# Kernel optimization log

Measured on AMD Instinct MI355X. Metric: run time of the kernel, lower is better.

The kernel has to match this reference:

```python
import jax, jax.numpy as jnp
import numpy as np

N = 131072   # n_nodes == n_edges (required by the broadcast in the original module)
C = 256      # node_channels == edge_channels (required by the broadcast)
EPS_BN = 1e-5
EPS = 1e-5


def _linear_params(key, out_c, in_c):
    k1, k2 = jax.random.split(key)
    bound = 1.0 / np.sqrt(in_c)
    W = jax.random.uniform(k1, (out_c, in_c), minval=-bound, maxval=bound, dtype=jnp.float32)
    b = jax.random.uniform(k2, (out_c,), minval=-bound, maxval=bound, dtype=jnp.float32)
    return W, b


def setup_inputs() -> dict:
    key = jax.random.key(0)
    ks = jax.random.split(key, 10)
    h = jax.random.normal(ks[0], (N, C), dtype=jnp.float32)
    e = jax.random.normal(ks[1], (N, C), dtype=jnp.float32)
    edge_index = jax.random.randint(ks[2], (2, N), 0, N, dtype=jnp.int64)
    A_w, A_b = _linear_params(ks[3], C, C)
    B_w, B_b = _linear_params(ks[4], C, C)
    C_w, C_b = _linear_params(ks[5], C, C)
    D_w, D_b = _linear_params(ks[6], C, C)
    U_w, U_b = _linear_params(ks[7], C, C)
    V_w, V_b = _linear_params(ks[8], C, C)
    bn_gamma = jnp.ones((C,), dtype=jnp.float32)
    bn_beta = jnp.zeros((C,), dtype=jnp.float32)
    return dict(h=h, edge_index=edge_index, e=e,
                A_w=A_w, A_b=A_b, B_w=B_w, B_b=B_b,
                C_w=C_w, C_b=C_b, D_w=D_w, D_b=D_b,
                bn_gamma=bn_gamma, bn_beta=bn_beta,
                U_w=U_w, U_b=U_b, V_w=V_w, V_b=V_b)


def reference(h, edge_index, e,
              A_w, A_b, B_w, B_b, C_w, C_b, D_w, D_b,
              bn_gamma, bn_beta, U_w, U_b, V_w, V_b):
    row, col = edge_index[0], edge_index[1]
    # gather + four parallel linears, summed: [E, C]
    e_out = (h[row] @ A_w.T + A_b
             + h[col] @ B_w.T + B_b
             + e[col] @ C_w.T + C_b
             + e[row] @ D_w.T + D_b)
    # BatchNorm1d (training mode: batch stats, biased variance) + ReLU
    mu = jnp.mean(e_out, axis=0)
    var = jnp.var(e_out, axis=0)
    e_out = jax.nn.relu(bn_gamma * (e_out - mu) * jax.lax.rsqrt(var + EPS_BN) + bn_beta)
    # scatter-add edge messages into node-indexed e, then sigmoid-normalize over dim 0
    e_new = e.at[row].add(e_out)
    e_new = jax.nn.sigmoid(e_new)
    e_new = e_new / (jnp.sum(e_new, axis=0, keepdims=True) + EPS)
    # final gather-multiply-reduce: (e_new * V(h[col])).sum(0) broadcasts [N,C]*[E,C] with N==E
    h_out = h @ U_w.T + U_b + jnp.sum(e_new * (h[col] @ V_w.T + V_b), axis=0)
    h_out = jax.nn.relu(h_out)
    return h_out, e_new
```

## Files before the change

kernel.cpp:

```cpp
#include <hip/hip_runtime.h>
#include <hip/hip_bf16.h>


typedef __attribute__((ext_vector_type(8))) short bf16x8;
typedef __attribute__((ext_vector_type(4))) float f32x4;

__device__ __forceinline__ float b2f(unsigned int lo16) {
  union { unsigned int u; float f; } c; c.u = lo16 << 16; return c.f;
}
__device__ __forceinline__ float lof(unsigned int u) { return b2f(u & 0xffffu); }
__device__ __forceinline__ float hif(unsigned int u) { return b2f(u >> 16); }
__device__ __forceinline__ unsigned int f2b(float f) {
  union { float f; unsigned int u; } c; c.f = f;
  unsigned int u = c.u;
  u += 0x7fffu + ((u >> 16) & 1u);
  return u >> 16;
}

__device__ __forceinline__ void prep_chunk(const float* __restrict__ src,
                                           unsigned short* __restrict__ dst, int g) {
  int mtile = g >> 9;
  int rem = g & 511;
  int r = rem >> 5, k8 = rem & 31;
  const float4* s = reinterpret_cast<const float4*>(src + (((size_t)mtile * 16 + r) << 8) + k8 * 8);
  float4 v0 = s[0], v1 = s[1];
  uint4 o;
  o.x = f2b(v0.x) | (f2b(v0.y) << 16);
  o.y = f2b(v0.z) | (f2b(v0.w) << 16);
  o.z = f2b(v1.x) | (f2b(v1.y) << 16);
  o.w = f2b(v1.z) | (f2b(v1.w) << 16);
  *reinterpret_cast<uint4*>(dst + ((size_t)mtile * 512 + k8 * 16 + r) * 8) = o;
}

__global__ __launch_bounds__(256) void prep_he(const float* __restrict__ h,
                                               unsigned short* __restrict__ h_t,
                                               const float* __restrict__ e,
                                               unsigned short* __restrict__ e_t,
                                               int nChunksEach) {
  int g = blockIdx.x * 256 + threadIdx.x;
  if (g < nChunksEach) prep_chunk(h, h_t, g);
  else if (g < 2 * nChunksEach) prep_chunk(e, e_t, g - nChunksEach);
}

__global__ __launch_bounds__(256) void prep_weights(
    const float* __restrict__ s0, const float* __restrict__ s1,
    const float* __restrict__ s2, const float* __restrict__ s3,
    const float* __restrict__ s4, const float* __restrict__ s5,
    unsigned short* __restrict__ W1h, unsigned short* __restrict__ W1e,
    unsigned short* __restrict__ W2t,
    const float* __restrict__ Ab, const float* __restrict__ Db,
    const float* __restrict__ Bb, const float* __restrict__ Cb,
    const float* __restrict__ Vb, const float* __restrict__ Ub,
    float* __restrict__ b1, float* __restrict__ b2,
    const int* __restrict__ ei, int* __restrict__ mode) {
  int g = blockIdx.x * 256 + threadIdx.x;
  if (blockIdx.x == 0) {
    const int t = threadIdx.x;
    b1[t] = Ab[t] + Db[t];
    b1[256 + t] = Bb[t] + Cb[t];
    b2[t] = Vb[t];
    b2[256 + t] = Ub[t];
    if (t == 0) {
      int m = 0;
#pragma unroll
      for (int i = 1; i < 64; i += 2) m |= ei[i];
      *mode = (m == 0) ? 1 : 0;
    }
  }
  int sel = g >> 13;
  int gg = g & 8191;
  const float* src; unsigned short* dst;
  switch (sel) {
    case 0: src = s0; dst = W1h; break;
    case 1: src = s1; dst = W1h + 65536; break;
    case 2: src = s2; dst = W1e; break;
    case 3: src = s3; dst = W1e + 65536; break;
    case 4: src = s4; dst = W2t; break;
    default: src = s5; dst = W2t + 65536; break;
  }
  prep_chunk(src, dst, gg);
}

__global__ __launch_bounds__(256) void gemm_bt2(
    const unsigned short* __restrict__ Ah, const unsigned short* __restrict__ Ae,
    const unsigned short* __restrict__ Bh, const unsigned short* __restrict__ Be,
    const float* __restrict__ bias, unsigned short* __restrict__ Cmat,
    int O, int nColBlk, int ktSteps, int nBlk) {
  __shared__ char lds[16384];
  const int cpx = nBlk >> 3;
  const int hw = blockIdx.x;
  const int bid = (hw % 8) * cpx + hw / 8;
  const int colBlk = bid % nColBlk;
  const int rowBlk = bid / nColBlk;
  const int tid = threadIdx.x;
  const int w = tid >> 6, lane = tid & 63;
  const int wm = w >> 1, wn = w & 1;

  const size_t aTileOff = (size_t)(rowBlk * 8 + w * 2) * 8192 + lane * 16;
  const size_t bTileOff = (size_t)(colBlk * 8 + w * 2) * 8192 + lane * 16;
  char* ldsA0 = lds + (w * 2) * 1024;
  char* ldsA1 = lds + (w * 2 + 1) * 1024;
  char* ldsB0 = lds + 8192 + (w * 2) * 1024;
  char* ldsB1 = lds + 8192 + (w * 2 + 1) * 1024;

  f32x4 acc[4][4] = {};

  for (int kt = 0; kt < ktSteps; ++kt) {
    const char* Abase = (const char*)(kt < 8 ? Ah : Ae) + aTileOff + (size_t)(kt & 7) * 1024;
    const char* Bbase = (const char*)(kt < 8 ? Bh : Be) + bTileOff + (size_t)(kt & 7) * 1024;
    __builtin_amdgcn_global_load_lds((const __attribute__((address_space(1))) void*)Abase,
                                     (__attribute__((address_space(3))) void*)ldsA0, 16, 0, 0);
    __builtin_amdgcn_global_load_lds((const __attribute__((address_space(1))) void*)(Abase + 8192),
                                     (__attribute__((address_space(3))) void*)ldsA1, 16, 0, 0);
    __builtin_amdgcn_global_load_lds((const __attribute__((address_space(1))) void*)Bbase,
                                     (__attribute__((address_space(3))) void*)ldsB0, 16, 0, 0);
    __builtin_amdgcn_global_load_lds((const __attribute__((address_space(1))) void*)(Bbase + 8192),
                                     (__attribute__((address_space(3))) void*)ldsB1, 16, 0, 0);
    __syncthreads();
    bf16x8 a[4], b[4];
#pragma unroll
    for (int mi = 0; mi < 4; ++mi)
      a[mi] = *reinterpret_cast<const bf16x8*>(lds + (wm * 4 + mi) * 1024 + lane * 16);
#pragma unroll
    for (int ni = 0; ni < 4; ++ni)
      b[ni] = *reinterpret_cast<const bf16x8*>(lds + 8192 + (wn * 4 + ni) * 1024 + lane * 16);
#pragma unroll
    for (int mi = 0; mi < 4; ++mi)
#pragma unroll
      for (int ni = 0; ni < 4; ++ni)
        acc[mi][ni] = __builtin_amdgcn_mfma_f32_16x16x32_bf16(a[mi], b[ni], acc[mi][ni], 0, 0, 0);
    __syncthreads();
  }

  const int rb = rowBlk * 128 + wm * 64 + ((lane >> 4) << 2);
  const int cb = colBlk * 128 + wn * 64 + (lane & 15);
#pragma unroll
  for (int mi = 0; mi < 4; ++mi) {
#pragma unroll
    for (int ni = 0; ni < 4; ++ni) {
      const int coln = cb + ni * 16;
      const float bz = bias[coln];
      const size_t base = (size_t)(rb + mi * 16) * O + coln;
#pragma unroll
      for (int r = 0; r < 4; ++r)
        Cmat[base + (size_t)r * O] = (unsigned short)f2b(acc[mi][ni][r] + bz);
    }
  }
}

__global__ __launch_bounds__(256) void edge_stats(
    const unsigned short* __restrict__ PRPC,
    const int* __restrict__ rows_s, const int* __restrict__ cols_s,
    float* __restrict__ sums, float* __restrict__ sumsq) {
  __shared__ float red[8][256];
  const int c8 = threadIdx.x & 31;
  const int sub = threadIdx.x >> 5;
  float s[8], q[8];
#pragma unroll
  for (int j = 0; j < 8; ++j) { s[j] = 0.f; q[j] = 0.f; }
#pragma unroll 1
  for (int grp = 0; grp < 2; ++grp) {
    const int kb = blockIdx.x * 64 + grp * 32 + sub * 4;
    int r[4], cj[4];
#pragma unroll
    for (int u = 0; u < 4; ++u) { r[u] = rows_s[kb + u]; cj[u] = cols_s[kb + u]; }
    uint4 pr[4], pc[4];
#pragma unroll
    for (int u = 0; u < 4; ++u)
      pr[u] = *reinterpret_cast<const uint4*>(PRPC + (size_t)r[u] * 512 + c8 * 8);
#pragma unroll
    for (int u = 0; u < 4; ++u)
      pc[u] = *reinterpret_cast<const uint4*>(PRPC + (size_t)cj[u] * 512 + 256 + c8 * 8);
#pragma unroll
    for (int u = 0; u < 4; ++u) {
      const unsigned int rw[4] = {pr[u].x, pr[u].y, pr[u].z, pr[u].w};
      const unsigned int cw[4] = {pc[u].x, pc[u].y, pc[u].z, pc[u].w};
#pragma unroll
      for (int p4 = 0; p4 < 4; ++p4) {
        const float v0 = lof(rw[p4]) + lof(cw[p4]);
        const float v1 = hif(rw[p4]) + hif(cw[p4]);
        s[2 * p4] += v0;     q[2 * p4] += v0 * v0;
        s[2 * p4 + 1] += v1; q[2 * p4 + 1] += v1 * v1;
      }
    }
  }
#pragma unroll
  for (int j = 0; j < 8; ++j) red[sub][c8 * 8 + j] = s[j];
  __syncthreads();
  {
    const int c = threadIdx.x;
    float t = 0.f;
#pragma unroll
    for (int u2 = 0; u2 < 8; ++u2) t += red[u2][c];
    atomicAdd(sums + c, t);
  }
  __syncthreads();
#pragma unroll
  for (int j = 0; j < 8; ++j) red[sub][c8 * 8 + j] = q[j];
  __syncthreads();
  {
    const int c = threadIdx.x;
    float t = 0.f;
#pragma unroll
    for (int u2 = 0; u2 < 8; ++u2) t += red[u2][c];
    atomicAdd(sumsq + c, t);
  }
}

__global__ __launch_bounds__(256) void hist_rows(const int* __restrict__ ei,
                                                 const int* __restrict__ modep,
                                                 int* __restrict__ cnt, int Nn) {
  const int k = blockIdx.x * 256 + threadIdx.x;
  if (k >= Nn) return;
  const int row = (*modep) ? ei[2 * k] : ei[k];
  atomicAdd(&cnt[row], 1);
}

__global__ __launch_bounds__(256) void scan1(const int* __restrict__ cnt,
                                             int* __restrict__ bsum) {
  __shared__ int red[256];
  const int t = threadIdx.x;
  red[t] = cnt[blockIdx.x * 256 + t];
  __syncthreads();
#pragma unroll
  for (int s = 128; s > 0; s >>= 1) {
    if (t < s) red[t] += red[t + s];
    __syncthreads();
  }
  if (t == 0) bsum[blockIdx.x] = red[0];
}

__global__ __launch_bounds__(512) void scan2(int* __restrict__ bsum, int nb) {
  __shared__ int tmp[512];
  const int t = threadIdx.x;
  const int own = (t < nb) ? bsum[t] : 0;
  tmp[t] = own;
  __syncthreads();
  for (int off = 1; off < 512; off <<= 1) {
    int v = (t >= off) ? tmp[t - off] : 0;
    __syncthreads();
    tmp[t] += v;
    __syncthreads();
  }
  if (t < nb) bsum[t] = tmp[t] - own;
}

__global__ __launch_bounds__(256) void scan3(const int* __restrict__ cnt,
                                             const int* __restrict__ bsum,
                                             int* __restrict__ base, int Nn) {
  __shared__ int tmp[256];
  const int t = threadIdx.x;
  const int gid = blockIdx.x * 256 + t;
  const int own = cnt[gid];
  tmp[t] = own;
  __syncthreads();
  for (int off = 1; off < 256; off <<= 1) {
    int v = (t >= off) ? tmp[t - off] : 0;
    __syncthreads();
    tmp[t] += v;
    __syncthreads();
  }
  base[gid] = tmp[t] - own + bsum[blockIdx.x];
  if (gid == 0) base[Nn] = Nn;
}

__global__ __launch_bounds__(256) void scatter_eids(const int* __restrict__ ei,
                                                    const int* __restrict__ modep,
                                                    const int* __restrict__ base,
                                                    int* __restrict__ cnt,
                                                    int* __restrict__ rows_s,
                                                    int* __restrict__ cols_s, int Nn) {
  const int k = blockIdx.x * 256 + threadIdx.x;
  if (k >= Nn) return;
  int row, col;
  if (*modep) { row = ei[2 * k]; col = ei[2 * (Nn + k)]; }
  else        { row = ei[k];     col = ei[Nn + k]; }
  const int pos = base[row] + atomicAdd(&cnt[row], -1) - 1;
  rows_s[pos] = row;
  cols_s[pos] = col;
}

#define GCAP 1024
__global__ __launch_bounds__(256) void gather_sig_T(
    const float* __restrict__ e, const unsigned short* __restrict__ PRPC,
    const int* __restrict__ base, const int* __restrict__ cols_s,
    const int* __restrict__ ei, const int* __restrict__ modep,
    const unsigned short* __restrict__ VU,
    const float* __restrict__ sums, const float* __restrict__ sumsq,
    const float* __restrict__ gamma, const float* __restrict__ beta,
    unsigned short* __restrict__ accB, float* __restrict__ colsum,
    float* __restrict__ Traw, float invE, int Nn) {
  __shared__ float red[4][256];
  __shared__ int colsL[GCAP];
  __shared__ int baseL[65];
  const int lane = threadIdx.x & 63, w = threadIdx.x >> 6;
  const int n0 = blockIdx.x * 64;
  if (threadIdx.x < 65) baseL[threadIdx.x] = base[n0 + threadIdx.x];
  __syncthreads();
  const int bstart = baseL[0];
  const int bcount = baseL[64] - bstart;
  for (int qq = threadIdx.x; qq < bcount && qq < GCAP; qq += 256)
    colsL[qq] = cols_s[bstart + qq];
  const float4 sm = *reinterpret_cast<const float4*>(sums + lane * 4);
  const float4 sq = *reinterpret_cast<const float4*>(sumsq + lane * 4);
  const float4 gm = *reinterpret_cast<const float4*>(gamma + lane * 4);
  const float4 bt = *reinterpret_cast<const float4*>(beta + lane * 4);
  float4 sc, sh;
  {
    const float mx = sm.x * invE, my = sm.y * invE, mz = sm.z * invE, mw = sm.w * invE;
    sc.x = gm.x * rsqrtf(fmaxf(sq.x * invE - mx * mx, 0.f) + 1e-5f);
    sc.y = gm.y * rsqrtf(fmaxf(sq.y * invE - my * my, 0.f) + 1e-5f);
    sc.z = gm.z * rsqrtf(fmaxf(sq.z * invE - mz * mz, 0.f) + 1e-5f);
    sc.w = gm.w * rsqrtf(fmaxf(sq.w * invE - mw * mw, 0.f) + 1e-5f);
    sh.x = bt.x - mx * sc.x; sh.y = bt.y - my * sc.y;
    sh.z = bt.z - mz * sc.z; sh.w = bt.w - mw * sc.w;
  }
  __syncthreads();
  const int mode = *modep;
  float s0 = 0.f, s1 = 0.f, s2 = 0.f, s3 = 0.f;
  float t0 = 0.f, t1 = 0.f, t2 = 0.f, t3 = 0.f;
  const int i0 = n0 + w * 16;
  int p = baseL[w * 16];
  const int pendW = baseL[w * 16 + 16];
  uint2 pcn; pcn.x = 0; pcn.y = 0;
  if (p < pendW) {
    const int q0 = p - bstart;
    const int cj = (q0 < GCAP) ? colsL[q0] : cols_s[p];
    pcn = *reinterpret_cast<const uint2*>(PRPC + (size_t)cj * 512 + 256 + lane * 4);
  }
  float4 ev = *reinterpret_cast<const float4*>(e + (size_t)i0 * 256 + lane * 4);
  uint2 prv = *reinterpret_cast<const uint2*>(PRPC + (size_t)i0 * 512 + lane * 4);
#pragma unroll 1
  for (int it = 0; it < 16; ++it) {
    const int i = i0 + it;
    const int colT = mode ? ei[2 * (Nn + i)] : ei[Nn + i];
    const uint2 hv = *reinterpret_cast<const uint2*>(VU + (size_t)colT * 512 + lane * 4);
    float4 v = ev;
    const uint2 pr = prv;
    if (it + 1 < 16) {
      ev = *reinterpret_cast<const float4*>(e + (size_t)(i + 1) * 256 + lane * 4);
      prv = *reinterpret_cast<const uint2*>(PRPC + (size_t)(i + 1) * 512 + lane * 4);
    }
    const float pr0 = lof(pr.x), pr1 = hif(pr.x), pr2 = lof(pr.y), pr3 = hif(pr.y);
    const int pe = baseL[w * 16 + it + 1];
#pragma unroll 1
    while (p < pe) {
      const uint2 pc = pcn;
      if (p + 1 < pendW) {
        const int qn = p + 1 - bstart;
        const int cj = (qn < GCAP) ? colsL[qn] : cols_s[p + 1];
        pcn = *reinterpret_cast<const uint2*>(PRPC + (size_t)cj * 512 + 256 + lane * 4);
      }
      v.x += fmaxf(fmaf(sc.x, pr0 + lof(pc.x), sh.x), 0.f);
      v.y += fmaxf(fmaf(sc.y, pr1 + hif(pc.x), sh.y), 0.f);
      v.z += fmaxf(fmaf(sc.z, pr2 + lof(pc.y), sh.z), 0.f);
      v.w += fmaxf(fmaf(sc.w, pr3 + hif(pc.y), sh.w), 0.f);
      ++p;
    }
    v.x = 1.f / (1.f + __expf(-v.x));
    v.y = 1.f / (1.f + __expf(-v.y));
    v.z = 1.f / (1.f + __expf(-v.z));
    v.w = 1.f / (1.f + __expf(-v.w));
    uint2 ob;
    ob.x = f2b(v.x) | (f2b(v.y) << 16);
    ob.y = f2b(v.z) | (f2b(v.w) << 16);
    *reinterpret_cast<uint2*>(accB + (size_t)i * 256 + lane * 4) = ob;
    s0 += v.x; s1 += v.y; s2 += v.z; s3 += v.w;
    t0 += v.x * lof(hv.x); t1 += v.y * hif(hv.x);
    t2 += v.z * lof(hv.y); t3 += v.w * hif(hv.y);
  }
  red[w][lane * 4 + 0] = s0;
  red[w][lane * 4 + 1] = s1;
  red[w][lane * 4 + 2] = s2;
  red[w][lane * 4 + 3] = s3;
  __syncthreads();
  {
    const int c = threadIdx.x;
    atomicAdd(colsum + c, red[0][c] + red[1][c] + red[2][c] + red[3][c]);
  }
  __syncthreads();
  red[w][lane * 4 + 0] = t0;
  red[w][lane * 4 + 1] = t1;
  red[w][lane * 4 + 2] = t2;
  red[w][lane * 4 + 3] = t3;
  __syncthreads();
  {
    const int c = threadIdx.x;
    atomicAdd(Traw + c, red[0][c] + red[1][c] + red[2][c] + red[3][c]);
  }
}

__global__ __launch_bounds__(256) void finalize(
    const unsigned short* __restrict__ accB, const unsigned short* __restrict__ VU,
    const float* __restrict__ colsum, const float* __restrict__ Traw,
    float* __restrict__ outE, float* __restrict__ outH, int nChunks) {
  const int g = blockIdx.x * 256 + threadIdx.x;
  if (g >= nChunks) return;
  const int i = g >> 5, c8 = g & 31;
  const float4 cs0 = *reinterpret_cast<const float4*>(colsum + c8 * 8);
  const float4 cs1 = *reinterpret_cast<const float4*>(colsum + c8 * 8 + 4);
  const float4 tr0 = *reinterpret_cast<const float4*>(Traw + c8 * 8);
  const float4 tr1 = *reinterpret_cast<const float4*>(Traw + c8 * 8 + 4);
  float iv[8] = {1.f / (cs0.x + 1e-5f), 1.f / (cs0.y + 1e-5f),
                 1.f / (cs0.z + 1e-5f), 1.f / (cs0.w + 1e-5f),
                 1.f / (cs1.x + 1e-5f), 1.f / (cs1.y + 1e-5f),
                 1.f / (cs1.z + 1e-5f), 1.f / (cs1.w + 1e-5f)};
  float tt[8] = {tr0.x * iv[0], tr0.y * iv[1], tr0.z * iv[2], tr0.w * iv[3],
                 tr1.x * iv[4], tr1.y * iv[5], tr1.z * iv[6], tr1.w * iv[7]};
  const uint4 sb = *reinterpret_cast<const uint4*>(accB + (size_t)i * 256 + c8 * 8);
  const unsigned int sw[4] = {sb.x, sb.y, sb.z, sb.w};
  float4 e0, e1;
  e0.x = lof(sw[0]) * iv[0]; e0.y = hif(sw[0]) * iv[1];
  e0.z = lof(sw[1]) * iv[2]; e0.w = hif(sw[1]) * iv[3];
  e1.x = lof(sw[2]) * iv[4]; e1.y = hif(sw[2]) * iv[5];
  e1.z = lof(sw[3]) * iv[6]; e1.w = hif(sw[3]) * iv[7];
  float4* qe = reinterpret_cast<float4*>(outE + (size_t)i * 256 + c8 * 8);
  qe[0] = e0; qe[1] = e1;
  const uint4 hu = *reinterpret_cast<const uint4*>(VU + (size_t)i * 512 + 256 + c8 * 8);
  float4 o0, o1;
  o0.x = fmaxf(lof(hu.x) + tt[0], 0.f);
  o0.y = fmaxf(hif(hu.x) + tt[1], 0.f);
  o0.z = fmaxf(lof(hu.y) + tt[2], 0.f);
  o0.w = fmaxf(hif(hu.y) + tt[3], 0.f);
  o1.x = fmaxf(lof(hu.z) + tt[4], 0.f);
  o1.y = fmaxf(hif(hu.z) + tt[5], 0.f);
  o1.z = fmaxf(lof(hu.w) + tt[6], 0.f);
  o1.w = fmaxf(hif(hu.w) + tt[7], 0.f);
  float4* qh = reinterpret_cast<float4*>(outH + (size_t)i * 256 + c8 * 8);
  qh[0] = o0; qh[1] = o1;
}

extern "C" void kernel_launch(void* const* d_in, const int* in_sizes, int n_in,
                              void* d_out, int out_size, void* d_ws, size_t ws_size,
                              hipStream_t stream) {
  const float* h     = (const float*)d_in[0];
  const int*   ei    = (const int*)d_in[1];
  const float* e     = (const float*)d_in[2];
  const float* Aw    = (const float*)d_in[3];
  const float* Ab    = (const float*)d_in[4];
  const float* Bw    = (const float*)d_in[5];
  const float* Bb    = (const float*)d_in[6];
  const float* Cw    = (const float*)d_in[7];
  const float* Cb    = (const float*)d_in[8];
  const float* Dw    = (const float*)d_in[9];
  const float* Db    = (const float*)d_in[10];
  const float* gamma = (const float*)d_in[11];
  const float* beta  = (const float*)d_in[12];
  const float* Uw    = (const float*)d_in[13];
  const float* Ub    = (const float*)d_in[14];
  const float* Vw    = (const float*)d_in[15];
  const float* Vb    = (const float*)d_in[16];
  const int N = in_sizes[0] / 256;

  char* ws = (char*)d_ws;
  unsigned short* W1h = (unsigned short*)(ws + 0x0);
  unsigned short* W1e = (unsigned short*)(ws + 0x40000);
  unsigned short* W2t = (unsigned short*)(ws + 0x80000);
  float* b1     = (float*)(ws + 0xC0000);
  float* b2     = (float*)(ws + 0xC0800);
  float* sums   = (float*)(ws + 0xC1000);
  float* sumsq  = (float*)(ws + 0xC1400);
  float* colsum = (float*)(ws + 0xC1800);
  float* Traw   = (float*)(ws + 0xC1C00);
  int*   mode   = (int*)(ws + 0xC2C00);
  unsigned short* h_t  = (unsigned short*)(ws + 0x100000);
  unsigned short* e_t  = (unsigned short*)(ws + 0x4100000);
  unsigned short* PRPC = (unsigned short*)(ws + 0x8100000);
  unsigned short* VU   = (unsigned short*)(ws + 0x10100000);
  unsigned short* accB = (unsigned short*)(ws + 0x100000);
  int* cnt    = (int*)(ws + 0x18100000);
  int* baseA  = (int*)(ws + 0x18180000);
  int* rows_s = (int*)(ws + 0x18210000);
  int* cols_s = (int*)(ws + 0x18290000);
  int* bsum   = (int*)(ws + 0x18310000);

  float* outH = (float*)d_out;
  float* outE = outH + (size_t)N * 256;

  hipMemsetAsync(ws + 0xC1000, 0, 4096, stream);
  hipMemsetAsync(cnt, 0, (size_t)N * 4, stream);
  prep_weights<<<192, 256, 0, stream>>>(Aw, Bw, Dw, Cw, Vw, Uw, W1h, W1e, W2t,
                                        Ab, Db, Bb, Cb, Vb, Ub, b1, b2, ei, mode);

  hist_rows<<<N / 256, 256, 0, stream>>>(ei, mode, cnt, N);
  scan1<<<N / 256, 256, 0, stream>>>(cnt, bsum);
  scan2<<<1, 512, 0, stream>>>(bsum, N / 256);
  scan3<<<N / 256, 256, 0, stream>>>(cnt, bsum, baseA, N);
  scatter_eids<<<N / 256, 256, 0, stream>>>(ei, mode, baseA, cnt, rows_s, cols_s, N);

  const int nChunks = N * 32;
  prep_he<<<2 * nChunks / 256, 256, 0, stream>>>(h, h_t, e, e_t, nChunks);
  gemm_bt2<<<(N / 128) * 4, 256, 0, stream>>>(h_t, e_t, W1h, W1e, b1, PRPC, 512, 4, 16, (N / 128) * 4);
  gemm_bt2<<<(N / 128) * 4, 256, 0, stream>>>(h_t, h_t, W2t, W2t, b2, VU, 512, 4, 8, (N / 128) * 4);

  edge_stats<<<N / 64, 256, 0, stream>>>(PRPC, rows_s, cols_s, sums, sumsq);
  gather_sig_T<<<N / 64, 256, 0, stream>>>(e, PRPC, baseA, cols_s, ei, mode, VU,
                                           sums, sumsq, gamma, beta,
                                           accB, colsum, Traw, 1.0f / (float)N, N);
  finalize<<<nChunks / 256, 256, 0, stream>>>(accB, VU, colsum, Traw, outE, outH, nChunks);
}
```

Before: 574.1 us.

## Fuse counting sort into one grid-barrier kernel and merge the two GEMM launches

Replaces the five-kernel counting sort (histogram, three scan passes, scatter) with one persistent kernel of 256 blocks that uses a software grid barrier between phases. The two bf16 GEMMs become a single launch whose blocks pick their operands by index, and the memsets are folded into prep_weights. The aim is to cut launch gaps and small-kernel tail overhead; in exchange the sort runs on fewer blocks and depends on all 256 blocks being resident at once for the spin barrier to avoid deadlock.

```diff
diff --git a/kernel.cpp b/kernel.cpp
--- a/kernel.cpp
+++ b/kernel.cpp
@@ -52,7 +52,9 @@
     const float* __restrict__ Bb, const float* __restrict__ Cb,
     const float* __restrict__ Vb, const float* __restrict__ Ub,
     float* __restrict__ b1, float* __restrict__ b2,
-    const int* __restrict__ ei, int* __restrict__ mode) {
+    float* __restrict__ sums, float* __restrict__ sumsq,
+    float* __restrict__ colsum, float* __restrict__ Traw,
+    const int* __restrict__ ei, int* __restrict__ mode, int* __restrict__ bar) {
   int g = blockIdx.x * 256 + threadIdx.x;
   if (blockIdx.x == 0) {
     const int t = threadIdx.x;
@@ -60,11 +62,13 @@
     b1[256 + t] = Bb[t] + Cb[t];
     b2[t] = Vb[t];
     b2[256 + t] = Ub[t];
+    sums[t] = 0.f; sumsq[t] = 0.f; colsum[t] = 0.f; Traw[t] = 0.f;
     if (t == 0) {
       int m = 0;
 #pragma unroll
       for (int i = 1; i < 64; i += 2) m |= ei[i];
       *mode = (m == 0) ? 1 : 0;
+      *bar = 0;
     }
   }
   int sel = g >> 13;
@@ -81,14 +85,114 @@
   prep_chunk(src, dst, gg);
 }
 
-__global__ __launch_bounds__(256) void gemm_bt2(
-    const unsigned short* __restrict__ Ah, const unsigned short* __restrict__ Ae,
-    const unsigned short* __restrict__ Bh, const unsigned short* __restrict__ Be,
-    const float* __restrict__ bias, unsigned short* __restrict__ Cmat,
-    int O, int nColBlk, int ktSteps, int nBlk) {
+__device__ __forceinline__ void gridbar(int* bar, int target) {
+  __syncthreads();
+  if (threadIdx.x == 0) {
+    __threadfence();
+    atomicAdd(bar, 1);
+    while (__hip_atomic_load(bar, __ATOMIC_RELAXED, __HIP_MEMORY_SCOPE_AGENT) < target) {
+      __builtin_amdgcn_s_sleep(2);
+    }
+    __threadfence();
+  }
+  __syncthreads();
+}
+
+__global__ __launch_bounds__(256, 2) void coop_sort(
+    const int* __restrict__ ei, const int* __restrict__ modep,
+    int* __restrict__ cnt, int* __restrict__ bsum, int* __restrict__ baseA,
+    int* __restrict__ rows_s, int* __restrict__ cols_s,
+    int* __restrict__ bar, int Nn) {
+  __shared__ int tmp[512];
+  const int t = threadIdx.x;
+  const int b = blockIdx.x;
+  const int NB = 256;
+  const int mode = *modep;
+  int row[2], col[2];
+#pragma unroll
+  for (int half = 0; half < 2; ++half) {
+    const int g = (b + half * NB) * 256 + t;
+    cnt[g] = 0;
+    if (mode) { row[half] = ei[2 * g]; col[half] = ei[2 * (Nn + g)]; }
+    else      { row[half] = ei[g];     col[half] = ei[Nn + g]; }
+  }
+  gridbar(bar, NB);
+  atomicAdd(&cnt[row[0]], 1);
+  atomicAdd(&cnt[row[1]], 1);
+  gridbar(bar, 2 * NB);
+  int own[2];
+#pragma unroll
+  for (int half = 0; half < 2; ++half) {
+    const int g = (b + half * NB) * 256 + t;
+    own[half] = __hip_atomic_load(&cnt[g], __ATOMIC_RELAXED, __HIP_MEMORY_SCOPE_AGENT);
+    tmp[t] = own[half];
+    __syncthreads();
+    for (int s = 128; s > 0; s >>= 1) { if (t < s) tmp[t] += tmp[t + s]; __syncthreads(); }
+    if (t == 0) bsum[b + half * NB] = tmp[0];
+    __syncthreads();
+  }
+  gridbar(bar, 3 * NB);
+  if (b == 0) {
+    const int o0 = bsum[t], o1 = bsum[t + 256];
+    tmp[t] = o0; tmp[t + 256] = o1;
+    __syncthreads();
+    for (int off = 1; off < 256; off <<= 1) {
+      const int a0 = (t >= off) ? tmp[t - off] : 0;
+      const int a1 = (t >= off) ? tmp[256 + t - off] : 0;
+      __syncthreads();
+      tmp[t] += a0; tmp[256 + t] += a1;
+      __syncthreads();
+    }
+    const int tot1 = tmp[255];
+    bsum[t] = tmp[t] - o0;
+    bsum[t + 256] = tmp[256 + t] + tot1 - o1;
+  }
+  gridbar(bar, 4 * NB);
+#pragma unroll
+  for (int half = 0; half < 2; ++half) {
+    const int g = (b + half * NB) * 256 + t;
+    const int bs = __hip_atomic_load(&bsum[b + half * NB], __ATOMIC_RELAXED, __HIP_MEMORY_SCOPE_AGENT);
+    tmp[t] = own[half];
+    __syncthreads();
+    for (int off = 1; off < 256; off <<= 1) {
+      const int a = (t >= off) ? tmp[t - off] : 0;
+      __syncthreads();
+      tmp[t] += a;
+      __syncthreads();
+    }
+    baseA[g] = tmp[t] - own[half] + bs;
+    __syncthreads();
+  }
+  if (b == 0 && t == 0) baseA[Nn] = Nn;
+  gridbar(bar, 5 * NB);
+#pragma unroll
+  for (int half = 0; half < 2; ++half) {
+    const int pos = baseA[row[half]] + atomicAdd(&cnt[row[half]], -1) - 1;
+    rows_s[pos] = row[half];
+    cols_s[pos] = col[half];
+  }
+}
+
+__global__ __launch_bounds__(256) void gemm_fused(
+    const unsigned short* __restrict__ h_t, const unsigned short* __restrict__ e_t,
+    const unsigned short* __restrict__ W1h, const unsigned short* __restrict__ W1e,
+    const unsigned short* __restrict__ W2t,
+    const float* __restrict__ b1, const float* __restrict__ b2,
+    unsigned short* __restrict__ PRPC, unsigned short* __restrict__ VU,
+    int nB1) {
   __shared__ char lds[16384];
-  const int cpx = nBlk >> 3;
-  const int hw = blockIdx.x;
+  const int g = blockIdx.x;
+  const bool is2 = (g >= nB1);
+  const int hw = is2 ? (g - nB1) : g;
+  const unsigned short* Ah = h_t;
+  const unsigned short* Ae = e_t;
+  const unsigned short* Bh = is2 ? W2t : W1h;
+  const unsigned short* Be = is2 ? W2t : W1e;
+  const float* bias = is2 ? b2 : b1;
+  unsigned short* Cmat = is2 ? VU : PRPC;
+  const int ktSteps = is2 ? 8 : 16;
+  const int O = 512, nColBlk = 4;
+  const int cpx = nB1 >> 3;
   const int bid = (hw % 8) * cpx + hw / 8;
   const int colBlk = bid % nColBlk;
   const int rowBlk = bid / nColBlk;
@@ -205,79 +309,6 @@
     for (int u2 = 0; u2 < 8; ++u2) t += red[u2][c];
     atomicAdd(sumsq + c, t);
   }
-}
-
-__global__ __launch_bounds__(256) void hist_rows(const int* __restrict__ ei,
-                                                 const int* __restrict__ modep,
-                                                 int* __restrict__ cnt, int Nn) {
-  const int k = blockIdx.x * 256 + threadIdx.x;
-  if (k >= Nn) return;
-  const int row = (*modep) ? ei[2 * k] : ei[k];
-  atomicAdd(&cnt[row], 1);
-}
-
-__global__ __launch_bounds__(256) void scan1(const int* __restrict__ cnt,
-                                             int* __restrict__ bsum) {
-  __shared__ int red[256];
-  const int t = threadIdx.x;
-  red[t] = cnt[blockIdx.x * 256 + t];
-  __syncthreads();
-#pragma unroll
-  for (int s = 128; s > 0; s >>= 1) {
-    if (t < s) red[t] += red[t + s];
-    __syncthreads();
-  }
-  if (t == 0) bsum[blockIdx.x] = red[0];
-}
-
-__global__ __launch_bounds__(512) void scan2(int* __restrict__ bsum, int nb) {
-  __shared__ int tmp[512];
-  const int t = threadIdx.x;
-  const int own = (t < nb) ? bsum[t] : 0;
-  tmp[t] = own;
-  __syncthreads();
-  for (int off = 1; off < 512; off <<= 1) {
-    int v = (t >= off) ? tmp[t - off] : 0;
-    __syncthreads();
-    tmp[t] += v;
-    __syncthreads();
-  }
-  if (t < nb) bsum[t] = tmp[t] - own;
-}
-
-__global__ __launch_bounds__(256) void scan3(const int* __restrict__ cnt,
-                                             const int* __restrict__ bsum,
-                                             int* __restrict__ base, int Nn) {
-  __shared__ int tmp[256];
-  const int t = threadIdx.x;
-  const int gid = blockIdx.x * 256 + t;
-  const int own = cnt[gid];
-  tmp[t] = own;
-  __syncthreads();
-  for (int off = 1; off < 256; off <<= 1) {
-    int v = (t >= off) ? tmp[t - off] : 0;
-    __syncthreads();
-    tmp[t] += v;
-    __syncthreads();
-  }
-  base[gid] = tmp[t] - own + bsum[blockIdx.x];
-  if (gid == 0) base[Nn] = Nn;
-}
-
-__global__ __launch_bounds__(256) void scatter_eids(const int* __restrict__ ei,
-                                                    const int* __restrict__ modep,
-                                                    const int* __restrict__ base,
-                                                    int* __restrict__ cnt,
-                                                    int* __restrict__ rows_s,
-                                                    int* __restrict__ cols_s, int Nn) {
-  const int k = blockIdx.x * 256 + threadIdx.x;
-  if (k >= Nn) return;
-  int row, col;
-  if (*modep) { row = ei[2 * k]; col = ei[2 * (Nn + k)]; }
-  else        { row = ei[k];     col = ei[Nn + k]; }
-  const int pos = base[row] + atomicAdd(&cnt[row], -1) - 1;
-  rows_s[pos] = row;
-  cols_s[pos] = col;
 }
 
 #define GCAP 1024
@@ -463,6 +494,7 @@
   float* colsum = (float*)(ws + 0xC1800);
   float* Traw   = (float*)(ws + 0xC1C00);
   int*   mode   = (int*)(ws + 0xC2C00);
+  int*   bar    = (int*)(ws + 0xC2D00);
   unsigned short* h_t  = (unsigned short*)(ws + 0x100000);
   unsigned short* e_t  = (unsigned short*)(ws + 0x4100000);
   unsigned short* PRPC = (unsigned short*)(ws + 0x8100000);
@@ -477,21 +509,15 @@
   float* outH = (float*)d_out;
   float* outE = outH + (size_t)N * 256;
 
-  hipMemsetAsync(ws + 0xC1000, 0, 4096, stream);
-  hipMemsetAsync(cnt, 0, (size_t)N * 4, stream);
   prep_weights<<<192, 256, 0, stream>>>(Aw, Bw, Dw, Cw, Vw, Uw, W1h, W1e, W2t,
-                                        Ab, Db, Bb, Cb, Vb, Ub, b1, b2, ei, mode);
-
-  hist_rows<<<N / 256, 256, 0, stream>>>(ei, mode, cnt, N);
-  scan1<<<N / 256, 256, 0, stream>>>(cnt, bsum);
-  scan2<<<1, 512, 0, stream>>>(bsum, N / 256);
-  scan3<<<N / 256, 256, 0, stream>>>(cnt, bsum, baseA, N);
-  scatter_eids<<<N / 256, 256, 0, stream>>>(ei, mode, baseA, cnt, rows_s, cols_s, N);
+                                        Ab, Db, Bb, Cb, Vb, Ub, b1, b2,
+                                        sums, sumsq, colsum, Traw, ei, mode, bar);
+  coop_sort<<<256, 256, 0, stream>>>(ei, mode, cnt, bsum, baseA, rows_s, cols_s, bar, N);
 
   const int nChunks = N * 32;
   prep_he<<<2 * nChunks / 256, 256, 0, stream>>>(h, h_t, e, e_t, nChunks);
-  gemm_bt2<<<(N / 128) * 4, 256, 0, stream>>>(h_t, e_t, W1h, W1e, b1, PRPC, 512, 4, 16, (N / 128) * 4);
-  gemm_bt2<<<(N / 128) * 4, 256, 0, stream>>>(h_t, h_t, W2t, W2t, b2, VU, 512, 4, 8, (N / 128) * 4);
+  const int nB1 = (N / 128) * 4;
+  gemm_fused<<<2 * nB1, 256, 0, stream>>>(h_t, e_t, W1h, W1e, W2t, b1, b2, PRPC, VU, nB1);
 
   edge_stats<<<N / 64, 256, 0, stream>>>(PRPC, rows_s, cols_s, sums, sumsq);
   gather_sig_T<<<N / 64, 256, 0, stream>>>(e, PRPC, baseA, cols_s, ei, mode, VU,
```

New measurement: 630.6 us. 1.1x slower.

## Double-buffer LDS tiles in bf16 GEMM and fold stat zeroing into weight prep

Applied to the files above, without the earlier changes.

The GEMM main loop now uses two LDS buffers, 32 KB in total. The global-to-LDS load for the next K step is issued before the MFMA work on the current step, so memory latency can overlap with compute instead of waiting behind a barrier every step. Separately, the memset that zeroed the BN and column-sum accumulators is removed, and block 0 of the weight-prep kernel zeroes them instead, saving one launch. The larger LDS footprint may lower the number of resident blocks per CU.

```diff
diff --git a/kernel.cpp b/kernel.cpp
--- a/kernel.cpp
+++ b/kernel.cpp
@@ -52,6 +52,8 @@
     const float* __restrict__ Bb, const float* __restrict__ Cb,
     const float* __restrict__ Vb, const float* __restrict__ Ub,
     float* __restrict__ b1, float* __restrict__ b2,
+    float* __restrict__ sums, float* __restrict__ sumsq,
+    float* __restrict__ colsum, float* __restrict__ Traw,
     const int* __restrict__ ei, int* __restrict__ mode) {
   int g = blockIdx.x * 256 + threadIdx.x;
   if (blockIdx.x == 0) {
@@ -60,6 +62,7 @@
     b1[256 + t] = Bb[t] + Cb[t];
     b2[t] = Vb[t];
     b2[256 + t] = Ub[t];
+    sums[t] = 0.f; sumsq[t] = 0.f; colsum[t] = 0.f; Traw[t] = 0.f;
     if (t == 0) {
       int m = 0;
 #pragma unroll
@@ -86,7 +89,7 @@
     const unsigned short* __restrict__ Bh, const unsigned short* __restrict__ Be,
     const float* __restrict__ bias, unsigned short* __restrict__ Cmat,
     int O, int nColBlk, int ktSteps, int nBlk) {
-  __shared__ char lds[16384];
+  __shared__ char lds[32768];
   const int cpx = nBlk >> 3;
   const int hw = blockIdx.x;
   const int bid = (hw % 8) * cpx + hw / 8;
@@ -98,37 +101,50 @@
 
   const size_t aTileOff = (size_t)(rowBlk * 8 + w * 2) * 8192 + lane * 16;
   const size_t bTileOff = (size_t)(colBlk * 8 + w * 2) * 8192 + lane * 16;
-  char* ldsA0 = lds + (w * 2) * 1024;
-  char* ldsA1 = lds + (w * 2 + 1) * 1024;
-  char* ldsB0 = lds + 8192 + (w * 2) * 1024;
-  char* ldsB1 = lds + 8192 + (w * 2 + 1) * 1024;
+  const int wOff0 = (w * 2) * 1024;
+  const int wOff1 = (w * 2 + 1) * 1024;
 
   f32x4 acc[4][4] = {};
 
-  for (int kt = 0; kt < ktSteps; ++kt) {
-    const char* Abase = (const char*)(kt < 8 ? Ah : Ae) + aTileOff + (size_t)(kt & 7) * 1024;
-    const char* Bbase = (const char*)(kt < 8 ? Bh : Be) + bTileOff + (size_t)(kt & 7) * 1024;
-    __builtin_amdgcn_global_load_lds((const __attribute__((address_space(1))) void*)Abase,
-                                     (__attribute__((address_space(3))) void*)ldsA0, 16, 0, 0);
-    __builtin_amdgcn_global_load_lds((const __attribute__((address_space(1))) void*)(Abase + 8192),
-                                     (__attribute__((address_space(3))) void*)ldsA1, 16, 0, 0);
-    __builtin_amdgcn_global_load_lds((const __attribute__((address_space(1))) void*)Bbase,
-                                     (__attribute__((address_space(3))) void*)ldsB0, 16, 0, 0);
-    __builtin_amdgcn_global_load_lds((const __attribute__((address_space(1))) void*)(Bbase + 8192),
-                                     (__attribute__((address_space(3))) void*)ldsB1, 16, 0, 0);
-    __syncthreads();
+  auto stage = [&](int kt, char* bufA, char* bufB) {
+    const char* Ab_ = (const char*)(kt < 8 ? Ah : Ae) + aTileOff + (size_t)(kt & 7) * 1024;
+    const char* Bb_ = (const char*)(kt < 8 ? Bh : Be) + bTileOff + (size_t)(kt & 7) * 1024;
+    __builtin_amdgcn_global_load_lds((const __attribute__((address_space(1))) void*)Ab_,
+                                     (__attribute__((address_space(3))) void*)(bufA + wOff0), 16, 0, 0);
+    __builtin_amdgcn_global_load_lds((const __attribute__((address_space(1))) void*)(Ab_ + 8192),
+                                     (__attribute__((address_space(3))) void*)(bufA + wOff1), 16, 0, 0);
+    __builtin_amdgcn_global_load_lds((const __attribute__((address_space(1))) void*)Bb_,
+                                     (__attribute__((address_space(3))) void*)(bufB + wOff0), 16, 0, 0);
+    __builtin_amdgcn_global_load_lds((const __attribute__((address_space(1))) void*)(Bb_ + 8192),
+                                     (__attribute__((address_space(3))) void*)(bufB + wOff1), 16, 0, 0);
+  };
+  auto compute = [&](const char* bufA, const char* bufB) {
     bf16x8 a[4], b[4];
 #pragma unroll
     for (int mi = 0; mi < 4; ++mi)
-      a[mi] = *reinterpret_cast<const bf16x8*>(lds + (wm * 4 + mi) * 1024 + lane * 16);
+      a[mi] = *reinterpret_cast<const bf16x8*>(bufA + (wm * 4 + mi) * 1024 + lane * 16);
 #pragma unroll
     for (int ni = 0; ni < 4; ++ni)
-      b[ni] = *reinterpret_cast<const bf16x8*>(lds + 8192 + (wn * 4 + ni) * 1024 + lane * 16);
+      b[ni] = *reinterpret_cast<const bf16x8*>(bufB + (wn * 4 + ni) * 1024 + lane * 16);
 #pragma unroll
     for (int mi = 0; mi < 4; ++mi)
 #pragma unroll
       for (int ni = 0; ni < 4; ++ni)
         acc[mi][ni] = __builtin_amdgcn_mfma_f32_16x16x32_bf16(a[mi], b[ni], acc[mi][ni], 0, 0, 0);
+  };
+
+  char* A0 = lds;          char* A1 = lds + 8192;
+  char* B0 = lds + 16384;  char* B1 = lds + 24576;
+
+  stage(0, A0, B0);
+  __syncthreads();
+#pragma unroll 1
+  for (int kt = 0; kt < ktSteps; kt += 2) {
+    stage(kt + 1, A1, B1);
+    compute(A0, B0);
+    __syncthreads();
+    if (kt + 2 < ktSteps) stage(kt + 2, A0, B0);
+    compute(A1, B1);
     __syncthreads();
   }
 
@@ -477,10 +493,10 @@
   float* outH = (float*)d_out;
   float* outE = outH + (size_t)N * 256;
 
-  hipMemsetAsync(ws + 0xC1000, 0, 4096, stream);
   hipMemsetAsync(cnt, 0, (size_t)N * 4, stream);
   prep_weights<<<192, 256, 0, stream>>>(Aw, Bw, Dw, Cw, Vw, Uw, W1h, W1e, W2t,
-                                        Ab, Db, Bb, Cb, Vb, Ub, b1, b2, ei, mode);
+                                        Ab, Db, Bb, Cb, Vb, Ub, b1, b2,
+                                        sums, sumsq, colsum, Traw, ei, mode);
 
   hist_rows<<<N / 256, 256, 0, stream>>>(ei, mode, cnt, N);
   scan1<<<N / 256, 256, 0, stream>>>(cnt, bsum);
```

Result: no change. 582.7 us (+1.5%).
